# Kernel optimization log

Hardware: AMD Instinct MI355X
Metric: run time of the kernel (lower is better)

The kernel has to match this reference:

```python
import math
import jax, jax.numpy as jnp
from jax import lax
import numpy as np

C, H, W, N, K = 256, 64, 64, 16, 7

def setup_inputs() -> dict:
    key = jax.random.key(0)
    k0, k1, k2, k3, k4 = jax.random.split(key, 5)
    x = jax.random.normal(k0, (N, C, H, W), dtype=jnp.float32)
    p_2_w = 0.02 * jax.random.normal(k1, (1, C, H, 1), dtype=jnp.float32)
    # nn.Conv2d(c, c, (1,5), groups=1, bias=False) -> weight [c, c, 1, 5]
    fan_in = C * 1 * 5
    bound = 1.0 / math.sqrt(fan_in)
    p_3_w = jax.random.uniform(k2, (C, C, 1, 5), dtype=jnp.float32, minval=-bound, maxval=bound)
    p_4_w = 0.02 * jax.random.normal(k3, (1, C, K, 1, 1), dtype=jnp.float32)
    p_6_w = jax.random.uniform(k4, (K, 1), dtype=jnp.float32, minval=-7.0, maxval=7.0)
    return {"x": x, "p_2_w": p_2_w, "p_3_w": p_3_w, "p_4_w": p_4_w, "p_6_w": p_6_w}

def reference(x, p_2_w, p_3_w, p_4_w, p_6_w):
    n, c, h, w = x.shape
    k = p_4_w.shape[2]  # 7 taps
    pad = (k - 1) // 2
    # F.unfold with kernel (1,7), pad (0,3): stack 7 width-shifted copies -> [n,c,7,h,w]
    xp = jnp.pad(x, ((0, 0), (0, 0), (0, 0), (pad, pad)))
    t_1 = jnp.stack([xp[..., i:i + w] for i in range(k)], axis=2)
    # per-(channel,row) scaling then dense 1x5 conv
    t_2 = p_2_w * x
    t_3 = lax.conv_general_dilated(
        t_2, p_3_w, window_strides=(1, 1), padding=[(0, 0), (2, 2)],
        dimension_numbers=("NCHW", "OIHW", "NCHW"))
    # weighted tap-sum: (p_4_w * t_1) contracted over taps with p_6_w[:,0]
    t_4 = p_4_w * t_1
    t_6 = jnp.einsum("nckhw,kf->ncfhw", t_4, p_6_w)[:, :, 0]  # [n,c,h,w]
    t_5 = jax.nn.relu(x)
    s = h * w
    # channel-attention matrix [n,c,c]
    t_7 = jnp.einsum("ncs,nds->ncd", t_3.reshape(n, c, s), t_6.reshape(n, c, s))
    t_7 = t_7 * (1.0 / math.sqrt(s))
    # bmm(t_5^T, t_7) -> [n,s,d]; permuting to [n,d,h,w] == einsum 'ncs,ncd->nds'
    out = jnp.einsum("ncs,ncd->nds", t_5.reshape(n, c, s), t_7)
    out = out * (1.0 / math.sqrt(c))
    return out.reshape(n, c, h, w)
```

## Files before the change

kernel.cpp:

```cpp
#include <hip/hip_runtime.h>
#include <hip/hip_bf16.h>

typedef __attribute__((ext_vector_type(8))) short bf16x8;
typedef __attribute__((ext_vector_type(4))) float f32x4;

#define NB 16
#define CD 256
#define HD 64
#define WD 64
#define WP 68
#define SD 4096
#define KU 1280

__device__ __forceinline__ void gload16(const void* g, void* lds) {
  __builtin_amdgcn_global_load_lds(
      (const __attribute__((address_space(1))) unsigned int*)g,
      (__attribute__((address_space(3))) unsigned int*)lds, 16, 0, 0);
}

__global__ __launch_bounds__(256) void prep_x(const float* __restrict__ x,
                                              const float* __restrict__ p2,
                                              const float* __restrict__ p4,
                                              const float* __restrict__ p6,
                                              const float* __restrict__ p3,
                                              __hip_bfloat16* __restrict__ t2p,
                                              __hip_bfloat16* __restrict__ t5T,
                                              __hip_bfloat16* __restrict__ t6,
                                              __hip_bfloat16* __restrict__ A) {
  int h = blockIdx.x;
  int cb = blockIdx.y;
  int n = blockIdx.z;
  int c0 = cb * 64;
  __shared__ float xwp[64][76];
  __shared__ __hip_bfloat16 t5l[64][72];
  __shared__ __hip_bfloat16 t2l[64][72];
  int t = threadIdx.x;

  {
    int bid = (n * 64 + h) * 4 + cb;
    int id = bid * 256 + t;
    if (id < CD * KU) {
      int o = id / KU;
      int r = id - o * KU;
      int j = r >> 8;
      int c = r & 255;
      A[id] = __float2bfloat16(p3[(o * CD + c) * 5 + j]);
    }
  }

  {
    int r = t >> 2, cc = t & 3;
    xwp[r][cc] = 0.f;
    xwp[r][68 + cc] = 0.f;
  }

  {
    int w = t & 63, cg = (t >> 6) * 16;
    __hip_bfloat16 o5[16], o2[16];
#pragma unroll
    for (int j = 0; j < 16; ++j) {
      int c = c0 + cg + j;
      float xv = x[(((size_t)n * CD + c) * HD + h) * WD + w];
      float sc = p2[c * HD + h];
      xwp[cg + j][4 + w] = xv;
      o5[j] = __float2bfloat16(fmaxf(xv, 0.f));
      o2[j] = __float2bfloat16(sc * xv);
    }
    *reinterpret_cast<bf16x8*>(&t5l[w][cg]) = *reinterpret_cast<const bf16x8*>(&o5[0]);
    *reinterpret_cast<bf16x8*>(&t5l[w][cg + 8]) = *reinterpret_cast<const bf16x8*>(&o5[8]);
    *reinterpret_cast<bf16x8*>(&t2l[w][cg]) = *reinterpret_cast<const bf16x8*>(&o2[0]);
    *reinterpret_cast<bf16x8*>(&t2l[w][cg + 8]) = *reinterpret_cast<const bf16x8*>(&o2[8]);
  }
  __syncthreads();

  __hip_bfloat16* t2pn = t2p + (size_t)n * HD * WP * CD;

  {
    int ws = t >> 2, ch = (t & 3) * 16;
    bf16x8 v0 = *reinterpret_cast<const bf16x8*>(&t5l[ws][ch]);
    bf16x8 v1 = *reinterpret_cast<const bf16x8*>(&t5l[ws][ch + 8]);
    size_t s = (size_t)h * 64 + ws;
    *reinterpret_cast<bf16x8*>(&t5T[((size_t)n * SD + s) * CD + c0 + ch]) = v0;
    *reinterpret_cast<bf16x8*>(&t5T[((size_t)n * SD + s) * CD + c0 + ch + 8]) = v1;
    bf16x8 u0 = *reinterpret_cast<const bf16x8*>(&t2l[ws][ch]);
    bf16x8 u1 = *reinterpret_cast<const bf16x8*>(&t2l[ws][ch + 8]);
    *reinterpret_cast<bf16x8*>(&t2pn[((size_t)h * WP + ws + 2) * CD + c0 + ch]) = u0;
    *reinterpret_cast<bf16x8*>(&t2pn[((size_t)h * WP + ws + 2) * CD + c0 + ch + 8]) = u1;
  }
  if (t < 32) {
    int pi = t >> 3;
    int wp = (pi < 2) ? pi : pi + 64;
    int cc = (t & 7) * 8;
    bf16x8 z = (bf16x8){0, 0, 0, 0, 0, 0, 0, 0};
    *reinterpret_cast<bf16x8*>(&t2pn[((size_t)h * WP + wp) * CD + c0 + cc]) = z;
  }

  {
    int cl = t >> 2, w16 = (t & 3) * 16;
    float hx[24];
#pragma unroll
    for (int q = 0; q < 6; ++q) {
      float4 v = *reinterpret_cast<const float4*>(&xwp[cl][w16 + q * 4]);
      hx[q * 4 + 0] = v.x;
      hx[q * 4 + 1] = v.y;
      hx[q * 4 + 2] = v.z;
      hx[q * 4 + 3] = v.w;
    }
    float wt[7];
#pragma unroll
    for (int k = 0; k < 7; ++k) wt[k] = p4[(c0 + cl) * 7 + k] * p6[k];
    __hip_bfloat16 o6[16];
#pragma unroll
    for (int u = 0; u < 16; ++u) {
      float acc = 0.f;
#pragma unroll
      for (int k = 0; k < 7; ++k) acc += wt[k] * hx[u + 1 + k];
      o6[u] = __float2bfloat16(acc);
    }
    size_t base = ((size_t)n * CD + c0 + cl) * SD + h * 64 + w16;
    *reinterpret_cast<bf16x8*>(&t6[base]) = *reinterpret_cast<const bf16x8*>(&o6[0]);
    *reinterpret_cast<bf16x8*>(&t6[base + 8]) = *reinterpret_cast<const bf16x8*>(&o6[8]);
  }
}

#define VMWAIT(N) asm volatile("s_waitcnt vmcnt(" #N ")" ::: "memory")
#define BARRIER() __builtin_amdgcn_s_barrier()

#define ST4(kt, bi)                                                                    \
  do {                                                                                 \
    char* dst = lb + ((bi) << 15) + t * 16;                                            \
    gload16(gA0 + (kt) * 64, dst);                                                     \
    gload16(gA1 + (kt) * 64, dst + 8192);                                              \
    gload16(gB0 + (kt) * 64, dst + 16384);                                             \
    gload16(gB1 + (kt) * 64, dst + 24576);                                             \
  } while (0)

#define LDF(bi, AV, BV)                                                                \
  do {                                                                                 \
    const char* ba = lb + ((bi) << 15);                                                \
    _Pragma("unroll") for (int mf = 0; mf < 8; ++mf) {                                 \
      int row = wm * 128 + mf * 16 + l16;                                              \
      AV[mf] = *reinterpret_cast<const bf16x8*>(ba + row * 64 + ((lg ^ rxor) * 16));   \
    }                                                                                  \
    _Pragma("unroll") for (int nf = 0; nf < 4; ++nf) {                                 \
      int row = wn * 64 + nf * 16 + l16;                                               \
      BV[nf] = *reinterpret_cast<const bf16x8*>(ba + 16384 + row * 64 +                \
                                                ((lg ^ rxor) * 16));                   \
    }                                                                                  \
  } while (0)

#define MM(AV, BV)                                                                     \
  do {                                                                                 \
    __builtin_amdgcn_s_setprio(1);                                                     \
    _Pragma("unroll") for (int mf = 0; mf < 8; ++mf)                                   \
        _Pragma("unroll") for (int nf = 0; nf < 4; ++nf)                               \
            acc[mf][nf] = __builtin_amdgcn_mfma_f32_16x16x32_bf16(AV[mf], BV[nf],      \
                                                                  acc[mf][nf], 0, 0, 0); \
    __builtin_amdgcn_s_setprio(0);                                                     \
  } while (0)

__global__ __launch_bounds__(512, 2) void gemm_b8(const __hip_bfloat16* __restrict__ A,
                                                  const __hip_bfloat16* __restrict__ t2p,
                                                  __hip_bfloat16* __restrict__ t3) {
  __shared__ __align__(16) __hip_bfloat16 lds[65536];
  char* lb = (char*)lds;
  const int n = blockIdx.z;
  const int sb = blockIdx.x;
  const int t = threadIdx.x;
  const int wv = t >> 6, lane = t & 63;
  const int wm = wv >> 2, wn = wv & 3;
  const int l16 = lane & 15, lg = lane >> 4;
  const int s0 = sb * 256;
  const int rxor = (l16 >> 1) & 3;
  const char* Ab = (const char*)A;
  const char* t2pb = (const char*)(t2p + (size_t)n * HD * WP * CD);
  const int cbsrc = ((t & 3) ^ ((t >> 3) & 3)) * 16;

  const int r0 = t >> 2;
  const char* gA0 = Ab + (size_t)r0 * 2560 + cbsrc;
  const char* gA1 = Ab + (size_t)(r0 + 128) * 2560 + cbsrc;
  const int s1 = s0 + r0, s2 = s0 + r0 + 128;
  const char* gB0 = t2pb + (size_t)(s1 + 4 * (s1 >> 6)) * 512 + cbsrc;
  const char* gB1 = t2pb + (size_t)(s2 + 4 * (s2 >> 6)) * 512 + cbsrc;

  f32x4 acc[8][4];
#pragma unroll
  for (int i = 0; i < 8; ++i)
#pragma unroll
    for (int j = 0; j < 4; ++j) acc[i][j] = (f32x4){0.f, 0.f, 0.f, 0.f};

  bf16x8 avX[8], bvX[4], avY[8], bvY[4];

  ST4(0, 0);
  ST4(1, 1);
  ST4(2, 2);
  VMWAIT(4);
  BARRIER();
  LDF(0, avX, bvX);

  for (int k2 = 0; k2 < 18; ++k2) {
    const int kt = k2 * 2;
    ST4(kt + 3, (kt + 3) & 3);
    LDF((kt + 1) & 3, avY, bvY);
    MM(avX, bvX);
    VMWAIT(4);
    BARRIER();
    ST4(kt + 4, (kt + 4) & 3);
    LDF((kt + 2) & 3, avX, bvX);
    MM(avY, bvY);
    VMWAIT(4);
    BARRIER();
  }
  ST4(39, 3);
  LDF(1, avY, bvY);
  MM(avX, bvX);
  VMWAIT(4);
  BARRIER();
  LDF(2, avX, bvX);
  MM(avY, bvY);
  VMWAIT(0);
  BARRIER();
  LDF(3, avY, bvY);
  MM(avX, bvX);
  MM(avY, bvY);

  __hip_bfloat16* t3n = t3 + (size_t)n * CD * SD;
#pragma unroll
  for (int im = 0; im < 8; ++im)
#pragma unroll
    for (int in = 0; in < 4; ++in) {
      int row0 = wm * 128 + im * 16 + lg * 4;
      int col = s0 + wn * 64 + in * 16 + l16;
#pragma unroll
      for (int r = 0; r < 4; ++r)
        t3n[(size_t)(row0 + r) * SD + col] = __float2bfloat16(acc[im][in][r]);
    }
}

__global__ __launch_bounds__(256) void gemm_c_part(const __hip_bfloat16* __restrict__ t6,
                                                   const __hip_bfloat16* __restrict__ t3,
                                                   float* __restrict__ P4) {
  __shared__ __align__(16) __hip_bfloat16 lA[64 * 64];
  __shared__ __align__(16) __hip_bfloat16 lB[64 * 64];
  int bx = blockIdx.x;
  int cbk = bx & 3, kc = bx >> 2;
  int db = blockIdx.y;
  int n = blockIdx.z;
  int t = threadIdx.x;
  int wave = t >> 6, lane = t & 63;
  int wm = wave >> 1, wn = wave & 1;
  int l16 = lane & 15, lg = lane >> 4;
  int d0 = db * 64;
  int c0 = cbk * 64;
  int kbase = kc * 1024;
  const __hip_bfloat16* An = t6 + (size_t)n * CD * SD + kbase;
  const __hip_bfloat16* Bn = t3 + (size_t)n * CD * SD + kbase;

  int srow = t >> 3;
  int scol = (t & 7) * 8;
  const __hip_bfloat16* gA0 = An + (size_t)(d0 + srow) * SD + scol;
  const __hip_bfloat16* gA1 = An + (size_t)(d0 + srow + 32) * SD + scol;
  const __hip_bfloat16* gB0 = Bn + (size_t)(c0 + srow) * SD + scol;
  const __hip_bfloat16* gB1 = Bn + (size_t)(c0 + srow + 32) * SD + scol;
  __hip_bfloat16* lAd0 = &lA[t * 8];
  __hip_bfloat16* lAd1 = &lA[t * 8 + 32 * 64];
  __hip_bfloat16* lBd0 = &lB[t * 8];
  __hip_bfloat16* lBd1 = &lB[t * 8 + 32 * 64];

  f32x4 acc[2][2];
#pragma unroll
  for (int mi = 0; mi < 2; ++mi)
#pragma unroll
    for (int ni = 0; ni < 2; ++ni) acc[mi][ni] = (f32x4){0.f, 0.f, 0.f, 0.f};

  gload16(gA0, lAd0);
  gload16(gA1, lAd1);
  gload16(gB0, lBd0);
  gload16(gB1, lBd1);

  for (int k = 0; k < 16; ++k) {
    __syncthreads();
#pragma unroll
    for (int ks = 0; ks < 2; ++ks) {
      bf16x8 a[2], b[2];
#pragma unroll
      for (int mi = 0; mi < 2; ++mi)
        a[mi] = *reinterpret_cast<const bf16x8*>(&lA[(wm * 32 + mi * 16 + l16) * 64 + ks * 32 + lg * 8]);
#pragma unroll
      for (int ni = 0; ni < 2; ++ni)
        b[ni] = *reinterpret_cast<const bf16x8*>(&lB[(wn * 32 + ni * 16 + l16) * 64 + ks * 32 + lg * 8]);
#pragma unroll
      for (int mi = 0; mi < 2; ++mi)
#pragma unroll
        for (int ni = 0; ni < 2; ++ni)
          acc[mi][ni] = __builtin_amdgcn_mfma_f32_16x16x32_bf16(a[mi], b[ni], acc[mi][ni], 0, 0, 0);
    }
    __syncthreads();
    if (k < 15) {
      int kk = (k + 1) * 64;
      gload16(gA0 + kk, lAd0);
      gload16(gA1 + kk, lAd1);
      gload16(gB0 + kk, lBd0);
      gload16(gB1 + kk, lBd1);
    }
  }

  float* Pn = P4 + ((size_t)kc * NB + n) * CD * CD;
#pragma unroll
  for (int mi = 0; mi < 2; ++mi)
#pragma unroll
    for (int ni = 0; ni < 2; ++ni) {
      int col = c0 + wn * 32 + ni * 16 + l16;
      int row0 = d0 + wm * 32 + mi * 16 + lg * 4;
#pragma unroll
      for (int r = 0; r < 4; ++r)
        Pn[(size_t)(row0 + r) * CD + col] = acc[mi][ni][r];
    }
}

__global__ __launch_bounds__(256) void reduce_P(const float* __restrict__ P4,
                                                __hip_bfloat16* __restrict__ P) {
  size_t i = ((size_t)blockIdx.x * 256 + threadIdx.x) * 4;
  const size_t stride = (size_t)NB * CD * CD;
  float4 a = *reinterpret_cast<const float4*>(P4 + i);
  float4 b = *reinterpret_cast<const float4*>(P4 + stride + i);
  float4 c = *reinterpret_cast<const float4*>(P4 + 2 * stride + i);
  float4 d = *reinterpret_cast<const float4*>(P4 + 3 * stride + i);
  __hip_bfloat16 o[4];
  o[0] = __float2bfloat16((a.x + b.x + c.x + d.x) * 0.015625f);
  o[1] = __float2bfloat16((a.y + b.y + c.y + d.y) * 0.015625f);
  o[2] = __float2bfloat16((a.z + b.z + c.z + d.z) * 0.015625f);
  o[3] = __float2bfloat16((a.w + b.w + c.w + d.w) * 0.015625f);
  *reinterpret_cast<short4*>(&P[i]) = *reinterpret_cast<const short4*>(o);
}

#define DSTAGE_A(i, kk)                                                                \
  gload16(Pb + (size_t)((i) * 32 + wv4 * 8 + (lane >> 3)) * 512 + (kk) * 128 + cbsrc,  \
          (char*)lA + (i) * 4096 + wv4 * 1024)
#define DSTAGE_B(i, kk)                                                                \
  gload16(Tb + (size_t)(s0 + (i) * 32 + wv4 * 8 + (lane >> 3)) * 512 + (kk) * 128 + cbsrc, \
          (char*)lB + (i) * 4096 + wv4 * 1024)

__global__ __launch_bounds__(256, 2) void gemm_d(const __hip_bfloat16* __restrict__ P,
                                                 const __hip_bfloat16* __restrict__ t5T,
                                                 float* __restrict__ out) {
  __shared__ __align__(16) __hip_bfloat16 lA[256 * 64];
  __shared__ __align__(16) __hip_bfloat16 lB[128 * 64];
  const int n = blockIdx.z;
  const int sb = blockIdx.x;
  const int t = threadIdx.x;
  const int wv4 = t >> 6, lane = t & 63;
  const int wm = wv4 >> 1, wn = wv4 & 1;
  const int l16 = lane & 15, lg = lane >> 4;
  const int s0 = sb * 128;
  const char* Pb = (const char*)(P + (size_t)n * CD * CD);
  const char* Tb = (const char*)(t5T + (size_t)n * SD * CD);
  const int cbsrc = ((lane & 7) ^ (lane >> 3)) * 16;
  const int lxor = (l16 & 7) * 8;

  f32x4 acc[8][4];
#pragma unroll
  for (int i = 0; i < 8; ++i)
#pragma unroll
    for (int j = 0; j < 4; ++j) acc[i][j] = (f32x4){0.f, 0.f, 0.f, 0.f};

#pragma unroll
  for (int i = 0; i < 8; ++i) DSTAGE_A(i, 0);
#pragma unroll
  for (int i = 0; i < 4; ++i) DSTAGE_B(i, 0);

  for (int k = 0; k < 4; ++k) {
    __syncthreads();
#pragma unroll
    for (int ks = 0; ks < 2; ++ks) {
      int cb = (ks * 32 + lg * 8) ^ lxor;
      bf16x8 a[8], b[4];
#pragma unroll
      for (int mf = 0; mf < 8; ++mf)
        a[mf] = *reinterpret_cast<const bf16x8*>(&lA[(wm * 128 + mf * 16 + l16) * 64 + cb]);
#pragma unroll
      for (int nf = 0; nf < 4; ++nf)
        b[nf] = *reinterpret_cast<const bf16x8*>(&lB[(wn * 64 + nf * 16 + l16) * 64 + cb]);
#pragma unroll
      for (int mf = 0; mf < 8; ++mf)
#pragma unroll
        for (int nf = 0; nf < 4; ++nf)
          acc[mf][nf] = __builtin_amdgcn_mfma_f32_16x16x32_bf16(a[mf], b[nf], acc[mf][nf], 0, 0, 0);
    }
    __syncthreads();
    if (k < 3) {
      int kk = k + 1;
#pragma unroll
      for (int i = 0; i < 8; ++i) DSTAGE_A(i, kk);
#pragma unroll
      for (int i = 0; i < 4; ++i) DSTAGE_B(i, kk);
    }
  }

  float* outn = out + (size_t)n * CD * SD;
#pragma unroll
  for (int mf = 0; mf < 8; ++mf)
#pragma unroll
    for (int nf = 0; nf < 4; ++nf) {
      int col = s0 + wn * 64 + nf * 16 + l16;
      int row0 = wm * 128 + mf * 16 + lg * 4;
#pragma unroll
      for (int r = 0; r < 4; ++r)
        outn[(size_t)(row0 + r) * SD + col] = acc[mf][nf][r] * 0.0625f;
    }
}

extern "C" void kernel_launch(void* const* d_in, const int* in_sizes, int n_in,
                              void* d_out, int out_size, void* d_ws, size_t ws_size,
                              hipStream_t stream) {
  const float* x = (const float*)d_in[0];
  const float* p2 = (const float*)d_in[1];
  const float* p3 = (const float*)d_in[2];
  const float* p4 = (const float*)d_in[3];
  const float* p6 = (const float*)d_in[4];

  char* ws = (char*)d_ws;
  size_t off = 0;
  __hip_bfloat16* A = (__hip_bfloat16*)(ws + off);
  off += (size_t)CD * KU * 2;
  size_t t2p_off = off;
  __hip_bfloat16* t2p = (__hip_bfloat16*)(ws + off);
  off += (size_t)NB * HD * WP * CD * 2;
  __hip_bfloat16* t5T = (__hip_bfloat16*)(ws + off);
  off += (size_t)NB * SD * CD * 2;
  __hip_bfloat16* t6 = (__hip_bfloat16*)(ws + off);
  off += (size_t)NB * CD * SD * 2;
  __hip_bfloat16* t3 = (__hip_bfloat16*)(ws + off);
  off += (size_t)NB * CD * SD * 2;
  float* P4 = (float*)(ws + t2p_off);
  __hip_bfloat16* P = (__hip_bfloat16*)(ws + t2p_off + (size_t)4 * NB * CD * CD * 4);

  float* out = (float*)d_out;

  prep_x<<<dim3(HD, 4, NB), 256, 0, stream>>>(x, p2, p4, p6, p3, t2p, t5T, t6, A);
  gemm_b8<<<dim3(16, 1, NB), 512, 0, stream>>>(A, t2p, t3);
  gemm_c_part<<<dim3(16, 4, NB), 256, 0, stream>>>(t6, t3, P4);
  reduce_P<<<dim3((NB * CD * CD / 4) / 256), 256, 0, stream>>>(P4, P);
  gemm_d<<<dim3(32, 1, NB), 256, 0, stream>>>(P, t5T, out);
}
```

Measured before the change: 131.2 us.

## Halve gemm_b8 spatial tile and use double-buffered LDS to raise occupancy

```diff
diff --git a/kernel.cpp b/kernel.cpp
--- a/kernel.cpp
+++ b/kernel.cpp
@@ -126,20 +126,19 @@
 #define VMWAIT(N) asm volatile("s_waitcnt vmcnt(" #N ")" ::: "memory")
 #define BARRIER() __builtin_amdgcn_s_barrier()
 
-#define ST4(kt, bi)                                                                    \
+#define ST3(kt, bi)                                                                    \
   do {                                                                                 \
-    char* dst = lb + ((bi) << 15) + t * 16;                                            \
-    gload16(gA0 + (kt) * 64, dst);                                                     \
-    gload16(gA1 + (kt) * 64, dst + 8192);                                              \
-    gload16(gB0 + (kt) * 64, dst + 16384);                                             \
-    gload16(gB1 + (kt) * 64, dst + 24576);                                             \
+    char* dst = lb + (bi) * 24576 + t * 16;                                            \
+    gload16(gA0 + (kt) * 64, dst);                                \
+    gload16(gA1 + (kt) * 64, dst + 8192);                         \
+    gload16(gB0 + (kt) * 64, dst + 16384);                        \
   } while (0)
 
 #define LDF(bi, AV, BV)                                                                \
   do {                                                                                 \
-    const char* ba = lb + ((bi) << 15);                                                \
-    _Pragma("unroll") for (int mf = 0; mf < 8; ++mf) {                                 \
-      int row = wm * 128 + mf * 16 + l16;                                              \
+    const char* ba = lb + (bi) * 24576;                                                \
+    _Pragma("unroll") for (int mf = 0; mf < 4; ++mf) {                                 \
+      int row = wm * 64 + mf * 16 + l16;                                               \
       AV[mf] = *reinterpret_cast<const bf16x8*>(ba + row * 64 + ((lg ^ rxor) * 16));   \
     }                                                                                  \
     _Pragma("unroll") for (int nf = 0; nf < 4; ++nf) {                                 \
@@ -152,25 +151,25 @@
 #define MM(AV, BV)                                                                     \
   do {                                                                                 \
     __builtin_amdgcn_s_setprio(1);                                                     \
-    _Pragma("unroll") for (int mf = 0; mf < 8; ++mf)                                   \
+    _Pragma("unroll") for (int mf = 0; mf < 4; ++mf)                                   \
         _Pragma("unroll") for (int nf = 0; nf < 4; ++nf)                               \
             acc[mf][nf] = __builtin_amdgcn_mfma_f32_16x16x32_bf16(AV[mf], BV[nf],      \
                                                                   acc[mf][nf], 0, 0, 0); \
     __builtin_amdgcn_s_setprio(0);                                                     \
   } while (0)
 
-__global__ __launch_bounds__(512, 2) void gemm_b8(const __hip_bfloat16* __restrict__ A,
+__global__ __launch_bounds__(512, 4) void gemm_b8(const __hip_bfloat16* __restrict__ A,
                                                   const __hip_bfloat16* __restrict__ t2p,
                                                   __hip_bfloat16* __restrict__ t3) {
-  __shared__ __align__(16) __hip_bfloat16 lds[65536];
+  __shared__ __align__(16) __hip_bfloat16 lds[24576];
   char* lb = (char*)lds;
   const int n = blockIdx.z;
   const int sb = blockIdx.x;
   const int t = threadIdx.x;
   const int wv = t >> 6, lane = t & 63;
-  const int wm = wv >> 2, wn = wv & 3;
+  const int wm = wv >> 1, wn = wv & 1;
   const int l16 = lane & 15, lg = lane >> 4;
-  const int s0 = sb * 256;
+  const int s0 = sb * 128;
   const int rxor = (l16 >> 1) & 3;
   const char* Ab = (const char*)A;
   const char* t2pb = (const char*)(t2p + (size_t)n * HD * WP * CD);
@@ -179,61 +178,42 @@
   const int r0 = t >> 2;
   const char* gA0 = Ab + (size_t)r0 * 2560 + cbsrc;
   const char* gA1 = Ab + (size_t)(r0 + 128) * 2560 + cbsrc;
-  const int s1 = s0 + r0, s2 = s0 + r0 + 128;
+  const int s1 = s0 + r0;
   const char* gB0 = t2pb + (size_t)(s1 + 4 * (s1 >> 6)) * 512 + cbsrc;
-  const char* gB1 = t2pb + (size_t)(s2 + 4 * (s2 >> 6)) * 512 + cbsrc;
-
-  f32x4 acc[8][4];
-#pragma unroll
-  for (int i = 0; i < 8; ++i)
+
+  f32x4 acc[4][4];
+#pragma unroll
+  for (int i = 0; i < 4; ++i)
 #pragma unroll
     for (int j = 0; j < 4; ++j) acc[i][j] = (f32x4){0.f, 0.f, 0.f, 0.f};
 
-  bf16x8 avX[8], bvX[4], avY[8], bvY[4];
-
-  ST4(0, 0);
-  ST4(1, 1);
-  ST4(2, 2);
-  VMWAIT(4);
-  BARRIER();
-  LDF(0, avX, bvX);
-
-  for (int k2 = 0; k2 < 18; ++k2) {
-    const int kt = k2 * 2;
-    ST4(kt + 3, (kt + 3) & 3);
-    LDF((kt + 1) & 3, avY, bvY);
-    MM(avX, bvX);
-    VMWAIT(4);
-    BARRIER();
-    ST4(kt + 4, (kt + 4) & 3);
-    LDF((kt + 2) & 3, avX, bvX);
-    MM(avY, bvY);
-    VMWAIT(4);
-    BARRIER();
-  }
-  ST4(39, 3);
-  LDF(1, avY, bvY);
-  MM(avX, bvX);
-  VMWAIT(4);
-  BARRIER();
-  LDF(2, avX, bvX);
-  MM(avY, bvY);
+  bf16x8 av[4], bv[4];
+
+  ST3(0, 0);
   VMWAIT(0);
   BARRIER();
-  LDF(3, avY, bvY);
-  MM(avX, bvX);
-  MM(avY, bvY);
+
+  for (int kt = 0; kt < 40; ++kt) {
+    const int cur = kt & 1;
+    if (kt < 39) ST3(kt + 1, cur ^ 1);
+    LDF(cur, av, bv);
+    MM(av, bv);
+    if (kt < 39) {
+      VMWAIT(0);
+      BARRIER();
+    }
+  }
 
   __hip_bfloat16* t3n = t3 + (size_t)n * CD * SD;
 #pragma unroll
-  for (int im = 0; im < 8; ++im)
-#pragma unroll
-    for (int in = 0; in < 4; ++in) {
-      int row0 = wm * 128 + im * 16 + lg * 4;
-      int col = s0 + wn * 64 + in * 16 + l16;
+  for (int mf = 0; mf < 4; ++mf)
+#pragma unroll
+    for (int nf = 0; nf < 4; ++nf) {
+      int row0 = wm * 64 + mf * 16 + lg * 4;
+      int col = s0 + wn * 64 + nf * 16 + l16;
 #pragma unroll
       for (int r = 0; r < 4; ++r)
-        t3n[(size_t)(row0 + r) * SD + col] = __float2bfloat16(acc[im][in][r]);
+        t3n[(size_t)(row0 + r) * SD + col] = __float2bfloat16(acc[mf][nf][r]);
     }
 }
 
@@ -438,7 +418,7 @@
   float* out = (float*)d_out;
 
   prep_x<<<dim3(HD, 4, NB), 256, 0, stream>>>(x, p2, p4, p6, p3, t2p, t5T, t6, A);
-  gemm_b8<<<dim3(16, 1, NB), 512, 0, stream>>>(A, t2p, t3);
+  gemm_b8<<<dim3(32, 1, NB), 512, 0, stream>>>(A, t2p, t3);
   gemm_c_part<<<dim3(16, 4, NB), 256, 0, stream>>>(t6, t3, P4);
   reduce_P<<<dim3((NB * CD * CD / 4) / 256), 256, 0, stream>>>(P4, P);
   gemm_d<<<dim3(32, 1, NB), 256, 0, stream>>>(P, t5T, out);
```

New measurement: 135.2 us. 3.0% more time.
